# Optimization experiments

Hardware: AMD Instinct MI355X
Metric: run time of the kernel (lower is better)

Reference implementation:

```python
import jax, jax.numpy as jnp
import numpy as np

N = 100000   # nodes
E = 1600000  # edges per view
F = 256      # feature_dim
G = 512      # num graphs in batch
H, C = 2, 32 # heads, channels per head (GATConv(F, 32, heads=2))
EPS = 1e-5


def setup_inputs() -> dict:
    key = jax.random.key(0)
    ks = jax.random.split(key, 32)
    def w(i, shape, fan_in):
        return jax.random.normal(ks[i], shape, jnp.float32) / np.sqrt(fan_in)
    inp = {
        "x": jax.random.normal(ks[0], (N, F), jnp.float32),
        "edge_index_ast": jax.random.randint(ks[1], (2, E), 0, N),
        "edge_index_cfg": jax.random.randint(ks[2], (2, E), 0, N),
        "edge_index_pdg": jax.random.randint(ks[3], (2, E), 0, N),
        "batch": jnp.sort(jax.random.randint(ks[4], (N,), 0, G)),
        "num_graphs": G,
        # BatchNorm1d(feature_dim) affine params (training-mode batch stats)
        "bn_w": jnp.ones((F,), jnp.float32),
        "bn_b": jnp.zeros((F,), jnp.float32),
    }
    i = 5
    for v in ("ast", "cfg", "pdg"):
        inp[f"{v}_W"] = w(i, (F, H * C), F); i += 1
        inp[f"{v}_att_src"] = w(i, (H, C), C); i += 1
        inp[f"{v}_att_dst"] = w(i, (H, C), C); i += 1
        inp[f"{v}_bias"] = jnp.zeros((H * C,), jnp.float32)
    inp["g1_w"] = w(i, (64, 32), 64); i += 1
    inp["g1_b"] = jnp.zeros((32,), jnp.float32)
    inp["g2_w"] = w(i, (32, 3), 32); i += 1
    inp["g2_b"] = jnp.zeros((3,), jnp.float32)
    inp["c1_w"] = w(i, (64, 128), 64); i += 1
    inp["c1_b"] = jnp.zeros((128,), jnp.float32)
    inp["c2_w"] = w(i, (128, 64), 128); i += 1
    inp["c2_b"] = jnp.zeros((64,), jnp.float32)
    inp["c3_w"] = w(i, (64, 1), 64); i += 1
    inp["c3_b"] = jnp.zeros((1,), jnp.float32)
    return inp


def _gat(x, edge_index, W, att_src, att_dst, bias):
    """PyG GATConv (shared lin, add_self_loops=True, concat heads)."""
    n = x.shape[0]
    loops = jnp.arange(n)
    src = jnp.concatenate([edge_index[0], loops])
    dst = jnp.concatenate([edge_index[1], loops])
    h = (x @ W).reshape(n, H, C)                       # [N,H,C]
    a_src = jnp.sum(h * att_src, axis=-1)              # [N,H]
    a_dst = jnp.sum(h * att_dst, axis=-1)              # [N,H]
    e = jax.nn.leaky_relu(a_src[src] + a_dst[dst], 0.2)  # [Etot,H]
    m = jax.ops.segment_max(e, dst, num_segments=n)
    p = jnp.exp(e - m[dst])
    denom = jax.ops.segment_sum(p, dst, num_segments=n)
    alpha = p / (denom[dst] + 1e-16)                   # [Etot,H]
    out = jax.ops.segment_sum(h[src] * alpha[:, :, None], dst, num_segments=n)
    return out.reshape(n, H * C) + bias


def reference(x, edge_index_ast, edge_index_cfg, edge_index_pdg, batch, num_graphs,
              bn_w, bn_b,
              ast_W, ast_att_src, ast_att_dst, ast_bias,
              cfg_W, cfg_att_src, cfg_att_dst, cfg_bias,
              pdg_W, pdg_att_src, pdg_att_dst, pdg_bias,
              g1_w, g1_b, g2_w, g2_b,
              c1_w, c1_b, c2_w, c2_b, c3_w, c3_b):
    # input BatchNorm1d (training-mode batch statistics, biased variance)
    mu = x.mean(0)
    var = x.var(0)
    xn = (x - mu) / jnp.sqrt(var + EPS) * bn_w + bn_b

    h_ast = jax.ops.segment_max(jax.nn.elu(_gat(xn, edge_index_ast, ast_W, ast_att_src, ast_att_dst, ast_bias)), batch, num_segments=num_graphs)
    h_cfg = jax.ops.segment_max(jax.nn.elu(_gat(xn, edge_index_cfg, cfg_W, cfg_att_src, cfg_att_dst, cfg_bias)), batch, num_segments=num_graphs)
    h_pdg = jax.ops.segment_max(jax.nn.elu(_gat(xn, edge_index_pdg, pdg_W, pdg_att_src, pdg_att_dst, pdg_bias)), batch, num_segments=num_graphs)

    avg_view = (h_ast + h_cfg + h_pdg) / 3.0
    wts = jax.nn.softmax(jax.nn.relu(avg_view @ g1_w + g1_b) @ g2_w + g2_b, axis=-1)
    fused = wts[:, 0:1] * h_ast + wts[:, 1:2] * h_cfg + wts[:, 2:3] * h_pdg

    # classifier (dropout = identity at inference)
    z = jax.nn.relu(fused @ c1_w + c1_b)
    z = jax.nn.relu(z @ c2_w + c2_b)
    logits = (z @ c3_w + c3_b).reshape(-1)             # [G]
    return logits
```

## Files before the change

kernel.cpp:

```cpp
#include <hip/hip_runtime.h>
#include <hip/hip_bf16.h>
#include <hip/hip_fp16.h>

#define N_NODES 100000
#define N_EDGES 1600000
#define ETOT    (N_EDGES + N_NODES)
#define NE3     (3 * ETOT)
#define N3      (3 * N_NODES)
#define NF      256
#define NG      512
#define NHC     64
#define NOUT3   192
#define BN_EPS  1e-5f

#define NBUCK   586
#define NB1     1024
#define EGRAIN  20
#define ECHUNK  (256 * EGRAIN)
#define SCAN_N  (NBUCK * NB1)
#define ATT_NB  (N3 * 16 / 256)

typedef _Float16 f16x8 __attribute__((ext_vector_type(8)));
typedef float    f32x4 __attribute__((ext_vector_type(4)));

__device__ __forceinline__ unsigned fenc(float f){
  unsigned b = __float_as_uint(f);
  return (b & 0x80000000u) ? ~b : (b | 0x80000000u);
}
__device__ __forceinline__ float fdec(unsigned u){
  unsigned b = (u & 0x80000000u) ? (u & 0x7FFFFFFFu) : ~u;
  return __uint_as_float(b);
}
__device__ __forceinline__ float lrelu(float x){ return x > 0.f ? x : 0.2f * x; }
__device__ __forceinline__ float eluf(float x){ return x > 0.f ? x : (__expf(x) - 1.f); }

__global__ void k_init_pooled(unsigned* pooled){
  int i = blockIdx.x * 256 + threadIdx.x;
  if (i < 3 * NG * NHC) pooled[i] = 0x007FFFFFu;
}

#define STATS_NB ((N_NODES + 127) / 128)
__global__ __launch_bounds__(256) void k_pre(const float* __restrict__ x,
                                             float* __restrict__ sums, float* __restrict__ sumsq,
                                             const int* __restrict__ eA, const int* __restrict__ eC,
                                             const int* __restrict__ eP,
                                             int* __restrict__ gcounts){
  int t = threadIdx.x;
  if (blockIdx.x < STATS_NB){
    int r0 = blockIdx.x * 128;
    int rmax = N_NODES - r0; if (rmax > 128) rmax = 128;
    float s = 0.f, q = 0.f;
    for (int r = 0; r < rmax; ++r){
      float v = x[(size_t)(r0 + r) * NF + t];
      s += v; q += v * v;
    }
    atomicAdd(&sums[t], s);
    atomicAdd(&sumsq[t], q);
    return;
  }
  __shared__ int hist[NBUCK];
  int bi = blockIdx.x - STATS_NB;
  for (int b = t; b < NBUCK; b += 256) hist[b] = 0;
  __syncthreads();
  int base = bi * ECHUNK + t;
#pragma unroll
  for (int k = 0; k < EGRAIN; ++k){
    int i = base + k * 256;
    if (i < NE3){
      int v = i / ETOT; int j = i - v * ETOT;
      const int* ei = (v == 0) ? eA : (v == 1) ? eC : eP;
      int d = (j < N_EDGES) ? ei[N_EDGES + j] : (j - N_EDGES);
      int vd = v * N_NODES + d;
      atomicAdd(&hist[vd >> 9], 1);
    }
  }
  __syncthreads();
  for (int b = t; b < NBUCK; b += 256) gcounts[b * NB1 + bi] = hist[b];
}

__global__ __launch_bounds__(256) void k_prep2(const float* __restrict__ sums, const float* __restrict__ sumsq,
                                               const float* __restrict__ bn_w, const float* __restrict__ bn_b,
                                               const float* __restrict__ WA, const float* __restrict__ WC,
                                               const float* __restrict__ WP,
                                               __half* __restrict__ WpT, float* __restrict__ bp){
  __shared__ float red[256];
  int o = blockIdx.x;
  int v = o >> 6, oc = o & 63;
  const float* W = (v == 0) ? WA : (v == 1) ? WC : WP;
  int f = threadIdx.x;
  float mu  = sums[f]  * (1.f / N_NODES);
  float var = sumsq[f] * (1.f / N_NODES) - mu * mu;
  float sc  = bn_w[f] * rsqrtf(var + BN_EPS);
  float sh_ = bn_b[f] - mu * sc;
  float w = W[f * 64 + oc];
  WpT[(size_t)o * NF + f] = __float2half(w * sc);
  red[f] = sh_ * w;
  __syncthreads();
  for (int off = 128; off > 0; off >>= 1){
    if (f < off) red[f] += red[f + off];
    __syncthreads();
  }
  if (f == 0) bp[o] = red[0];
}

__global__ __launch_bounds__(256) void k_scan1(const int* __restrict__ cnt, int* __restrict__ out,
                                               int* __restrict__ bsum, int n){
  __shared__ int sh[256];
  int t = threadIdx.x; int base = blockIdx.x * 2048 + t * 8;
  int v[8]; int s = 0;
#pragma unroll
  for (int i = 0; i < 8; ++i){ v[i] = (base + i < n) ? cnt[base + i] : 0; s += v[i]; }
  sh[t] = s; __syncthreads();
  for (int off = 1; off < 256; off <<= 1){
    int xv = (t >= off) ? sh[t - off] : 0;
    __syncthreads();
    sh[t] += xv;
    __syncthreads();
  }
  int p = sh[t] - s;
  if (t == 255) bsum[blockIdx.x] = sh[255];
#pragma unroll
  for (int i = 0; i < 8; ++i){ if (base + i < n) out[base + i] = p; p += v[i]; }
}

__global__ __launch_bounds__(512) void k_scan2(int* __restrict__ bsum, int* __restrict__ total_out, int nb){
  __shared__ int sh[512];
  int t = threadIdx.x;
  int o = (t < nb) ? bsum[t] : 0;
  sh[t] = o; __syncthreads();
  for (int off = 1; off < 512; off <<= 1){
    int xv = (t >= off) ? sh[t - off] : 0;
    __syncthreads();
    sh[t] += xv;
    __syncthreads();
  }
  if (t < nb) bsum[t] = sh[t] - o;
  if (t == nb - 1) total_out[0] = sh[t];
}

__global__ __launch_bounds__(256) void k_scan3(int* __restrict__ out, const int* __restrict__ bsum, int n){
  int add = bsum[blockIdx.x];
  int base = blockIdx.x * 2048 + threadIdx.x * 8;
#pragma unroll
  for (int i = 0; i < 8; ++i) if (base + i < n) out[base + i] += add;
}

#define GBM 64
#define GEMM_NB ((N_NODES + GBM - 1) / GBM)
__global__ __launch_bounds__(256) void k_fused(const float* __restrict__ x,
                                               const __half* __restrict__ WpT, const float* __restrict__ bp,
                                               __half* __restrict__ h16,
                                               const int* __restrict__ eA, const int* __restrict__ eC,
                                               const int* __restrict__ eP,
                                               const int* __restrict__ gscan, int* __restrict__ packed){
  union U { _Float16 xs[64 * 256]; int pos[NBUCK]; };
  __shared__ U sm;
  int t = threadIdx.x;
  if (blockIdx.x >= GEMM_NB){
    int bi = blockIdx.x - GEMM_NB;
    for (int b = t; b < NBUCK; b += 256) sm.pos[b] = gscan[b * NB1 + bi];
    __syncthreads();
    int base = bi * ECHUNK + t;
#pragma unroll
    for (int k = 0; k < EGRAIN; ++k){
      int i = base + k * 256;
      if (i < NE3){
        int v = i / ETOT; int j = i - v * ETOT;
        const int* ei = (v == 0) ? eA : (v == 1) ? eC : eP;
        int s, d;
        if (j < N_EDGES){ s = ei[j]; d = ei[N_EDGES + j]; } else { s = j - N_EDGES; d = s; }
        int vd = v * N_NODES + d;
        int p = atomicAdd(&sm.pos[vd >> 9], 1);
        packed[p] = s | ((vd & 511) << 17);
      }
    }
    return;
  }
  int m0 = blockIdx.x * GBM;
#pragma unroll
  for (int k = 0; k < 8; ++k){
    int G = t + k * 256;
    int row = G >> 5, g = G & 31;
    int grow = m0 + row; if (grow >= N_NODES) grow = N_NODES - 1;
    const float4* src = (const float4*)(x + (size_t)grow * NF + ((g ^ (row & 7)) << 3));
    float4 lo = src[0], hi = src[1];
    f16x8 h;
    h[0]=(_Float16)lo.x; h[1]=(_Float16)lo.y; h[2]=(_Float16)lo.z; h[3]=(_Float16)lo.w;
    h[4]=(_Float16)hi.x; h[5]=(_Float16)hi.y; h[6]=(_Float16)hi.z; h[7]=(_Float16)hi.w;
    *(f16x8*)&sm.xs[(size_t)G << 3] = h;
  }
  __syncthreads();
  int lane = t & 63, w = t >> 6;
  int lr = lane & 15, lk = lane >> 4;
  int colb = w * 48;
  f32x4 acc[4][3];
#pragma unroll
  for (int mt = 0; mt < 4; ++mt)
#pragma unroll
    for (int ct = 0; ct < 3; ++ct) acc[mt][ct] = (f32x4){0.f, 0.f, 0.f, 0.f};
  float bpv[3];
#pragma unroll
  for (int ct = 0; ct < 3; ++ct) bpv[ct] = bp[colb + ct * 16 + lr];
#pragma unroll
  for (int kk = 0; kk < 8; ++kk){
    int khalf = kk * 32 + lk * 8;
    f16x8 av[4];
#pragma unroll
    for (int mt = 0; mt < 4; ++mt){
      int row = mt * 16 + lr;
      av[mt] = *(const f16x8*)&sm.xs[row * 256 + (khalf ^ ((row & 7) << 3))];
    }
    f16x8 bv[3];
#pragma unroll
    for (int ct = 0; ct < 3; ++ct){
      int col = colb + ct * 16 + lr;
      bv[ct] = *(const f16x8*)(const void*)(WpT + (size_t)col * NF + khalf);
    }
#pragma unroll
    for (int mt = 0; mt < 4; ++mt)
#pragma unroll
      for (int ct = 0; ct < 3; ++ct)
        acc[mt][ct] = __builtin_amdgcn_mfma_f32_16x16x32_f16(av[mt], bv[ct], acc[mt][ct], 0, 0, 0);
  }
#pragma unroll
  for (int mt = 0; mt < 4; ++mt){
#pragma unroll
    for (int r = 0; r < 4; ++r){
      int row = m0 + mt * 16 + lk * 4 + r;
      if (row < N_NODES){
#pragma unroll
        for (int ct = 0; ct < 3; ++ct)
          h16[(size_t)row * NOUT3 + colb + ct * 16 + lr] = __float2half(acc[mt][ct][r] + bpv[ct]);
      }
    }
  }
}

__global__ __launch_bounds__(256) void k_build(const int* __restrict__ gscan, const int* __restrict__ packed,
                                               int* __restrict__ entries, int* __restrict__ offsets){
  __shared__ int hist2[512];
  __shared__ int sh[256];
  int b = blockIdx.x, t = threadIdx.x;
  int base = gscan[b * NB1];
  int end  = (b == NBUCK - 1) ? NE3 : gscan[(b + 1) * NB1];
  hist2[t * 2] = 0; hist2[t * 2 + 1] = 0;
  __syncthreads();
  for (int i = base + t; i < end; i += 256)
    atomicAdd(&hist2[(packed[i] >> 17) & 511], 1);
  __syncthreads();
  int s0 = hist2[t * 2], s1 = hist2[t * 2 + 1];
  int tot = s0 + s1;
  sh[t] = tot; __syncthreads();
  for (int off = 1; off < 256; off <<= 1){
    int xv = (t >= off) ? sh[t - off] : 0;
    __syncthreads();
    sh[t] += xv;
    __syncthreads();
  }
  int p = sh[t] - tot;
  hist2[t * 2]     = p;
  hist2[t * 2 + 1] = p + s0;
  __syncthreads();
#pragma unroll
  for (int i = 0; i < 2; ++i){
    int vd = (b << 9) + t * 2 + i;
    if (vd < N3) offsets[vd] = base + hist2[t * 2 + i];
  }
  if (b == NBUCK - 1 && t == 0) offsets[N3] = NE3;
  __syncthreads();
  for (int i = base + t; i < end; i += 256){
    int pk = packed[i];
    int low = (pk >> 17) & 511;
    int pos = atomicAdd(&hist2[low], 1);
    entries[base + pos] = pk & 0x1FFFF;
  }
}

__global__ __launch_bounds__(256) void k_att(const __half* __restrict__ h16,
                                             const float* __restrict__ asA, const float* __restrict__ adA,
                                             const float* __restrict__ asC, const float* __restrict__ adC,
                                             const float* __restrict__ asP, const float* __restrict__ adP,
                                             float* __restrict__ a_src, float* __restrict__ a_dst,
                                             unsigned* __restrict__ gpart){
  __shared__ unsigned samax[6];
  int t = threadIdx.x;
  if (t < 6) samax[t] = 0u;
  __syncthreads();
  int gt = blockIdx.x * 256 + t;
  int g = gt >> 4; int lid = gt & 15;
  int v = g / N_NODES; int n = g - v * N_NODES;
  const float* As = (v == 0) ? asA : (v == 1) ? asC : asP;
  const float* Ad = (v == 0) ? adA : (v == 1) ? adC : adP;
  const __half2* hp = (const __half2*)(h16 + (size_t)n * NOUT3 + v * 64 + lid * 4);
  float2 fa = __half22float2(hp[0]);
  float2 fb = __half22float2(hp[1]);
  float4 s4 = *(const float4*)(As + lid * 4);
  float4 d4 = *(const float4*)(Ad + lid * 4);
  float rs = fa.x*s4.x + fa.y*s4.y + fb.x*s4.z + fb.y*s4.w;
  float rd = fa.x*d4.x + fa.y*d4.y + fb.x*d4.z + fb.y*d4.w;
  rs += __shfl_xor(rs, 1); rd += __shfl_xor(rd, 1);
  rs += __shfl_xor(rs, 2); rd += __shfl_xor(rd, 2);
  rs += __shfl_xor(rs, 4); rd += __shfl_xor(rd, 4);
  if ((lid & 7) == 0){
    int h = lid >> 3;
    a_src[g * 2 + h] = rs;
    a_dst[g * 2 + h] = rd;
    atomicMax(&samax[v * 2 + h], fenc(rs));
  }
  __syncthreads();
  if (t < 6) gpart[blockIdx.x * 6 + t] = samax[t];
}

__global__ __launch_bounds__(256) void k_amax(const unsigned* __restrict__ gpart, unsigned* __restrict__ amax){
  __shared__ unsigned sm[6];
  int t = threadIdx.x;
  if (t < 6) sm[t] = 0u;
  __syncthreads();
  unsigned m[6] = {0u, 0u, 0u, 0u, 0u, 0u};
  for (int bi = t; bi < ATT_NB; bi += 256){
    const unsigned* p = gpart + (size_t)bi * 6;
#pragma unroll
    for (int k = 0; k < 6; ++k) m[k] = max(m[k], p[k]);
  }
#pragma unroll
  for (int k = 0; k < 6; ++k) atomicMax(&sm[k], m[k]);
  __syncthreads();
  if (t < 6) amax[t] = sm[t];
}

__global__ __launch_bounds__(256) void k_gather(const int* __restrict__ entries, const int* __restrict__ offsets,
                                                const float* __restrict__ a_src, const float* __restrict__ a_dst,
                                                const unsigned* __restrict__ amax,
                                                const __half* __restrict__ h16,
                                                const float* __restrict__ bA, const float* __restrict__ bC,
                                                const float* __restrict__ bP,
                                                const int* __restrict__ batch, unsigned* __restrict__ pooled){
  __shared__ unsigned red[64];
  __shared__ int kmin, kmax;
  int t = threadIdx.x;
  if (t == 0){ kmin = 0x7FFFFFFF; kmax = -1; }
  if (t < 64) red[t] = 0u;
  __syncthreads();
  int grp = t >> 4;
  int lid = t & 15;
  int g = blockIdx.x * 16 + grp;
  int v = g / N_NODES; int n = g - v * N_NODES;
  int vN = v * N_NODES;
  float ad0 = a_dst[g*2+0], ad1 = a_dst[g*2+1];
  float m0 = lrelu(fdec(amax[v*2+0]) + ad0);
  float m1 = lrelu(fdec(amax[v*2+1]) + ad1);
  int beg = offsets[g], end = offsets[g+1];
  int len = end - beg;
  float ax = 0.f, ay = 0.f, az = 0.f, aw = 0.f;
  float den0 = 0.f, den1 = 0.f;
  const __half* hbase = h16 + v * 64 + lid * 4;
  for (int c0 = 0; c0 < len; c0 += 16){
    int nc = len - c0; if (nc > 16) nc = 16;
    int s_ = 0; float p0 = 0.f, p1 = 0.f;
    if (lid < nc){
      s_ = entries[beg + c0 + lid];
      float2 ap = *(const float2*)(a_src + (size_t)(vN + s_) * 2);
      p0 = __expf(lrelu(ap.x + ad0) - m0);
      p1 = __expf(lrelu(ap.y + ad1) - m1);
    }
    den0 += p0; den1 += p1;
    for (int k = 0; k < nc; k += 4){
      uint2 r[4]; float pav[4], pbv[4];
#pragma unroll
      for (int j = 0; j < 4; ++j){
        int kk = k + j;
        int sk = __shfl(s_, kk, 16);
        r[j] = *(const uint2*)(hbase + (size_t)sk * NOUT3);
        pav[j] = __shfl(p0, kk, 16);
        pbv[j] = __shfl(p1, kk, 16);
      }
#pragma unroll
      for (int j = 0; j < 4; ++j){
        int kk = k + j;
        if (kk < nc){
          float ph = (lid < 8) ? pav[j] : pbv[j];
          float2 fa2 = __half22float2(*(__half2*)&r[j].x);
          float2 fb2 = __half22float2(*(__half2*)&r[j].y);
          ax += ph * fa2.x; ay += ph * fa2.y; az += ph * fb2.x; aw += ph * fb2.y;
        }
      }
    }
  }
#pragma unroll
  for (int msk = 1; msk < 16; msk <<= 1){
    den0 += __shfl_xor(den0, msk);
    den1 += __shfl_xor(den1, msk);
  }
  float den = ((lid < 8) ? den0 : den1) + 1e-16f;
  const float* bias = (v == 0) ? bA : (v == 1) ? bC : bP;
  float4 b4 = *(const float4*)(bias + lid * 4);
  unsigned e0u = fenc(eluf(ax / den + b4.x));
  unsigned e1u = fenc(eluf(ay / den + b4.y));
  unsigned e2u = fenc(eluf(az / den + b4.z));
  unsigned e3u = fenc(eluf(aw / den + b4.w));
  int key = v * NG + batch[n];
  if (lid == 0){ atomicMin(&kmin, key); atomicMax(&kmax, key); }
  atomicMax(&red[lid*4+0], e0u); atomicMax(&red[lid*4+1], e1u);
  atomicMax(&red[lid*4+2], e2u); atomicMax(&red[lid*4+3], e3u);
  __syncthreads();
  if (kmin == kmax){
    if (t < 64) atomicMax(&pooled[(size_t)kmin * 64 + t], red[t]);
  } else {
    unsigned* pp = pooled + (size_t)key * 64 + lid * 4;
    atomicMax(pp+0, e0u); atomicMax(pp+1, e1u); atomicMax(pp+2, e2u); atomicMax(pp+3, e3u);
  }
}

__global__ __launch_bounds__(64) void k_head(const unsigned* __restrict__ pooled,
                                             const float* __restrict__ g1w, const float* __restrict__ g1b,
                                             const float* __restrict__ g2w, const float* __restrict__ g2b,
                                             const float* __restrict__ c1w, const float* __restrict__ c1b,
                                             const float* __restrict__ c2w, const float* __restrict__ c2b,
                                             const float* __restrict__ c3w, const float* __restrict__ c3b,
                                             float* __restrict__ out){
  __shared__ float s1[64];
  __shared__ float s2[128];
  __shared__ float sw[3];
  int g = blockIdx.x, l = threadIdx.x;
  float ha = fdec(pooled[(size_t)g * 64 + l]);
  float hc = fdec(pooled[(size_t)(NG + g) * 64 + l]);
  float hp = fdec(pooled[(size_t)(2 * NG + g) * 64 + l]);
  s1[l] = (ha + hc + hp) * (1.f / 3.f);
  __syncthreads();
  float r1 = 0.f;
  if (l < 32){
    r1 = g1b[l];
    for (int i = 0; i < 64; ++i) r1 += s1[i] * g1w[i * 32 + l];
    r1 = fmaxf(r1, 0.f);
  }
  __syncthreads();
  if (l < 32) s2[l] = r1;
  __syncthreads();
  if (l < 3){
    float tv = g2b[l];
    for (int i = 0; i < 32; ++i) tv += s2[i] * g2w[i * 3 + l];
    sw[l] = tv;
  }
  __syncthreads();
  float t0 = sw[0], t1 = sw[1], t2 = sw[2];
  float mx = fmaxf(t0, fmaxf(t1, t2));
  float w0 = __expf(t0 - mx), w1 = __expf(t1 - mx), w2 = __expf(t2 - mx);
  float wsum = w0 + w1 + w2;
  float fused = (w0 * ha + w1 * hc + w2 * hp) / wsum;
  __syncthreads();
  s1[l] = fused;
  __syncthreads();
  float za = c1b[l], zb = c1b[64 + l];
  for (int i = 0; i < 64; ++i){
    float f = s1[i];
    za += f * c1w[i * 128 + l];
    zb += f * c1w[i * 128 + 64 + l];
  }
  za = fmaxf(za, 0.f); zb = fmaxf(zb, 0.f);
  s2[l] = za; s2[64 + l] = zb;
  __syncthreads();
  float z2 = c2b[l];
  for (int i = 0; i < 128; ++i) z2 += s2[i] * c2w[i * 64 + l];
  z2 = fmaxf(z2, 0.f);
  float prod = z2 * c3w[l];
  for (int off = 32; off > 0; off >>= 1) prod += __shfl_down(prod, off);
  if (l == 0) out[g] = prod + c3b[0];
}

extern "C" void kernel_launch(void* const* d_in, const int* in_sizes, int n_in,
                              void* d_out, int out_size, void* d_ws, size_t ws_size,
                              hipStream_t stream){
  const float* x    = (const float*)d_in[0];
  const int* eA     = (const int*)d_in[1];
  const int* eC     = (const int*)d_in[2];
  const int* eP     = (const int*)d_in[3];
  const int* batch  = (const int*)d_in[4];
  const float* bn_w = (const float*)d_in[6];
  const float* bn_b = (const float*)d_in[7];
  const float* WA   = (const float*)d_in[8];
  const float* asA  = (const float*)d_in[9];
  const float* adA  = (const float*)d_in[10];
  const float* bA   = (const float*)d_in[11];
  const float* WC   = (const float*)d_in[12];
  const float* asC  = (const float*)d_in[13];
  const float* adC  = (const float*)d_in[14];
  const float* bC   = (const float*)d_in[15];
  const float* WP   = (const float*)d_in[16];
  const float* asP  = (const float*)d_in[17];
  const float* adP  = (const float*)d_in[18];
  const float* bP   = (const float*)d_in[19];
  const float* g1w  = (const float*)d_in[20];
  const float* g1b  = (const float*)d_in[21];
  const float* g2w  = (const float*)d_in[22];
  const float* g2b  = (const float*)d_in[23];
  const float* c1w  = (const float*)d_in[24];
  const float* c1b  = (const float*)d_in[25];
  const float* c2w  = (const float*)d_in[26];
  const float* c2b  = (const float*)d_in[27];
  const float* c3w  = (const float*)d_in[28];
  const float* c3b  = (const float*)d_in[29];
  float* out = (float*)d_out;

  char* wptr = (char*)d_ws;
  auto alloc = [&](size_t bytes) -> void* {
    void* p = (void*)wptr;
    wptr += (bytes + 255) & ~(size_t)255;
    return p;
  };
  float*    sums    = (float*)   alloc((size_t)NF * 4);
  float*    sumsq   = (float*)   alloc((size_t)NF * 4);
  size_t zbytes = (size_t)(wptr - (char*)sums);
  int*      gcounts = (int*)     alloc((size_t)SCAN_N * 4);
  int*      gscan   = (int*)     alloc((size_t)SCAN_N * 4);
  int*      offsets = (int*)     alloc(((size_t)N3 + 1) * 4);
  __half*   WpT     = (__half*)  alloc((size_t)NOUT3 * NF * 2);
  float*    bp      = (float*)   alloc((size_t)NOUT3 * 4);
  __half*   h16     = (__half*)  alloc((size_t)N_NODES * NOUT3 * 2);
  float*    a_src   = (float*)   alloc((size_t)N3 * 2 * 4);
  float*    a_dst   = (float*)   alloc((size_t)N3 * 2 * 4);
  int*      packed  = (int*)     alloc((size_t)NE3 * 4);
  int*      entries = (int*)     alloc((size_t)NE3 * 4);
  unsigned* pooled  = (unsigned*)alloc((size_t)3 * NG * NHC * 4);
  unsigned* gpart   = (unsigned*)alloc((size_t)ATT_NB * 6 * 4);
  unsigned* amax    = (unsigned*)alloc((size_t)64 * 4);
  int*      bsum    = (int*)     alloc((size_t)512 * 4);
  int*      scrtot  = (int*)     alloc((size_t)64 * 4);

  hipMemsetAsync(sums, 0, zbytes, stream);
  k_init_pooled<<<(3 * NG * NHC + 255) / 256, 256, 0, stream>>>(pooled);
  k_pre<<<STATS_NB + NB1, 256, 0, stream>>>(x, sums, sumsq, eA, eC, eP, gcounts);
  k_prep2<<<NOUT3, 256, 0, stream>>>(sums, sumsq, bn_w, bn_b, WA, WC, WP, WpT, bp);
  int nb_sc = (SCAN_N + 2047) / 2048;
  k_scan1<<<nb_sc, 256, 0, stream>>>(gcounts, gscan, bsum, SCAN_N);
  k_scan2<<<1, 512, 0, stream>>>(bsum, scrtot, nb_sc);
  k_scan3<<<nb_sc, 256, 0, stream>>>(gscan, bsum, SCAN_N);
  k_fused<<<GEMM_NB + NB1, 256, 0, stream>>>(x, WpT, bp, h16, eA, eC, eP, gscan, packed);
  k_att<<<ATT_NB, 256, 0, stream>>>(h16, asA, adA, asC, adC, asP, adP, a_src, a_dst, gpart);
  k_amax<<<1, 256, 0, stream>>>(gpart, amax);
  k_build<<<NBUCK, 256, 0, stream>>>(gscan, packed, entries, offsets);
  k_gather<<<N3 / 16, 256, 0, stream>>>(entries, offsets, a_src, a_dst, amax, h16, bA, bC, bP, batch, pooled);
  k_head<<<NG, 64, 0, stream>>>(pooled, g1w, g1b, g2w, g2b, c1w, c1b, c2w, c2b, c3w, c3b, out);
}
```

Measured before the change: 377.5 us.

## Precompute edge softmax weights in CSR build and narrow gather to 8 lanes

The CSR build kernel now computes each edge's unnormalized attention weights for both heads, using a_src, a_dst and the global max. It stores them as packed fp16 next to the source index in an 8-byte entry. The gather kernel then skips the random a_src lookup and the exp work, and uses 8 lanes per destination node with 16-byte feature loads instead of 16 lanes with 8-byte loads. The trade-off is doubled edge-entry traffic, fp16 rounding of the attention weights, and the exp plus random a_src access moving into the build kernel.

```diff
diff --git a/kernel.cpp b/kernel.cpp
--- a/kernel.cpp
+++ b/kernel.cpp
@@ -233,46 +233,6 @@
           h16[(size_t)row * NOUT3 + colb + ct * 16 + lr] = __float2half(acc[mt][ct][r] + bpv[ct]);
       }
     }
-  }
-}
-
-__global__ __launch_bounds__(256) void k_build(const int* __restrict__ gscan, const int* __restrict__ packed,
-                                               int* __restrict__ entries, int* __restrict__ offsets){
-  __shared__ int hist2[512];
-  __shared__ int sh[256];
-  int b = blockIdx.x, t = threadIdx.x;
-  int base = gscan[b * NB1];
-  int end  = (b == NBUCK - 1) ? NE3 : gscan[(b + 1) * NB1];
-  hist2[t * 2] = 0; hist2[t * 2 + 1] = 0;
-  __syncthreads();
-  for (int i = base + t; i < end; i += 256)
-    atomicAdd(&hist2[(packed[i] >> 17) & 511], 1);
-  __syncthreads();
-  int s0 = hist2[t * 2], s1 = hist2[t * 2 + 1];
-  int tot = s0 + s1;
-  sh[t] = tot; __syncthreads();
-  for (int off = 1; off < 256; off <<= 1){
-    int xv = (t >= off) ? sh[t - off] : 0;
-    __syncthreads();
-    sh[t] += xv;
-    __syncthreads();
-  }
-  int p = sh[t] - tot;
-  hist2[t * 2]     = p;
-  hist2[t * 2 + 1] = p + s0;
-  __syncthreads();
-#pragma unroll
-  for (int i = 0; i < 2; ++i){
-    int vd = (b << 9) + t * 2 + i;
-    if (vd < N3) offsets[vd] = base + hist2[t * 2 + i];
-  }
-  if (b == NBUCK - 1 && t == 0) offsets[N3] = NE3;
-  __syncthreads();
-  for (int i = base + t; i < end; i += 256){
-    int pk = packed[i];
-    int low = (pk >> 17) & 511;
-    int pos = atomicAdd(&hist2[low], 1);
-    entries[base + pos] = pk & 0x1FFFF;
   }
 }
 
@@ -328,9 +288,62 @@
   if (t < 6) amax[t] = sm[t];
 }
 
-__global__ __launch_bounds__(256) void k_gather(const int* __restrict__ entries, const int* __restrict__ offsets,
-                                                const float* __restrict__ a_src, const float* __restrict__ a_dst,
-                                                const unsigned* __restrict__ amax,
+__global__ __launch_bounds__(256) void k_build(const int* __restrict__ gscan, const int* __restrict__ packed,
+                                               const float* __restrict__ a_src, const float* __restrict__ a_dst,
+                                               const unsigned* __restrict__ amax,
+                                               uint2* __restrict__ ep, int* __restrict__ offsets){
+  __shared__ int hist2[512];
+  __shared__ int sh[256];
+  __shared__ float sam[6];
+  int b = blockIdx.x, t = threadIdx.x;
+  if (t < 6) sam[t] = fdec(amax[t]);
+  int base = gscan[b * NB1];
+  int end  = (b == NBUCK - 1) ? NE3 : gscan[(b + 1) * NB1];
+  hist2[t * 2] = 0; hist2[t * 2 + 1] = 0;
+  __syncthreads();
+  for (int i = base + t; i < end; i += 256)
+    atomicAdd(&hist2[(packed[i] >> 17) & 511], 1);
+  __syncthreads();
+  int s0 = hist2[t * 2], s1 = hist2[t * 2 + 1];
+  int tot = s0 + s1;
+  sh[t] = tot; __syncthreads();
+  for (int off = 1; off < 256; off <<= 1){
+    int xv = (t >= off) ? sh[t - off] : 0;
+    __syncthreads();
+    sh[t] += xv;
+    __syncthreads();
+  }
+  int p = sh[t] - tot;
+  hist2[t * 2]     = p;
+  hist2[t * 2 + 1] = p + s0;
+  __syncthreads();
+#pragma unroll
+  for (int i = 0; i < 2; ++i){
+    int vd = (b << 9) + t * 2 + i;
+    if (vd < N3) offsets[vd] = base + hist2[t * 2 + i];
+  }
+  if (b == NBUCK - 1 && t == 0) offsets[N3] = NE3;
+  __syncthreads();
+  for (int i = base + t; i < end; i += 256){
+    int pk = packed[i];
+    int low = (pk >> 17) & 511;
+    int s = pk & 0x1FFFF;
+    int vd = (b << 9) + low;
+    int v = (vd >= 2 * N_NODES) ? 2 : (vd >= N_NODES) ? 1 : 0;
+    float2 ad = *(const float2*)(a_dst + (size_t)vd * 2);
+    float2 as = *(const float2*)(a_src + (size_t)(v * N_NODES + s) * 2);
+    float m0 = lrelu(sam[v * 2 + 0] + ad.x);
+    float m1 = lrelu(sam[v * 2 + 1] + ad.y);
+    float p0 = __expf(lrelu(as.x + ad.x) - m0);
+    float p1 = __expf(lrelu(as.y + ad.y) - m1);
+    unsigned pu = (unsigned)__half_as_ushort(__float2half(p0))
+                | ((unsigned)__half_as_ushort(__float2half(p1)) << 16);
+    int pos = atomicAdd(&hist2[low], 1);
+    ep[base + pos] = make_uint2((unsigned)s, pu);
+  }
+}
+
+__global__ __launch_bounds__(256) void k_gather(const uint2* __restrict__ ep, const int* __restrict__ offsets,
                                                 const __half* __restrict__ h16,
                                                 const float* __restrict__ bA, const float* __restrict__ bC,
                                                 const float* __restrict__ bP,
@@ -341,73 +354,70 @@
   if (t == 0){ kmin = 0x7FFFFFFF; kmax = -1; }
   if (t < 64) red[t] = 0u;
   __syncthreads();
-  int grp = t >> 4;
-  int lid = t & 15;
-  int g = blockIdx.x * 16 + grp;
+  int grp = t >> 3;
+  int lid = t & 7;
+  int g = blockIdx.x * 32 + grp;
   int v = g / N_NODES; int n = g - v * N_NODES;
-  int vN = v * N_NODES;
-  float ad0 = a_dst[g*2+0], ad1 = a_dst[g*2+1];
-  float m0 = lrelu(fdec(amax[v*2+0]) + ad0);
-  float m1 = lrelu(fdec(amax[v*2+1]) + ad1);
   int beg = offsets[g], end = offsets[g+1];
   int len = end - beg;
-  float ax = 0.f, ay = 0.f, az = 0.f, aw = 0.f;
+  float acc[8];
+#pragma unroll
+  for (int e2 = 0; e2 < 8; ++e2) acc[e2] = 0.f;
   float den0 = 0.f, den1 = 0.f;
-  const __half* hbase = h16 + v * 64 + lid * 4;
-  for (int c0 = 0; c0 < len; c0 += 16){
-    int nc = len - c0; if (nc > 16) nc = 16;
-    int s_ = 0; float p0 = 0.f, p1 = 0.f;
+  const __half* hbase = h16 + v * 64 + lid * 8;
+  for (int c0 = 0; c0 < len; c0 += 8){
+    int nc = len - c0; if (nc > 8) nc = 8;
+    int s_ = 0; unsigned pu_ = 0u;
     if (lid < nc){
-      s_ = entries[beg + c0 + lid];
-      float2 ap = *(const float2*)(a_src + (size_t)(vN + s_) * 2);
-      p0 = __expf(lrelu(ap.x + ad0) - m0);
-      p1 = __expf(lrelu(ap.y + ad1) - m1);
-    }
-    den0 += p0; den1 += p1;
+      uint2 e = ep[beg + c0 + lid];
+      s_ = (int)e.x; pu_ = e.y;
+    }
+    den0 += __half2float(__ushort_as_half((unsigned short)(pu_ & 0xFFFFu)));
+    den1 += __half2float(__ushort_as_half((unsigned short)(pu_ >> 16)));
     for (int k = 0; k < nc; k += 4){
-      uint2 r[4]; float pav[4], pbv[4];
+      f16x8 r[4]; float pa[4];
 #pragma unroll
       for (int j = 0; j < 4; ++j){
         int kk = k + j;
-        int sk = __shfl(s_, kk, 16);
-        r[j] = *(const uint2*)(hbase + (size_t)sk * NOUT3);
-        pav[j] = __shfl(p0, kk, 16);
-        pbv[j] = __shfl(p1, kk, 16);
+        int sk = __shfl(s_, kk, 8);
+        unsigned pk_ = (unsigned)__shfl((int)pu_, kk, 8);
+        r[j] = *(const f16x8*)(hbase + (size_t)sk * NOUT3);
+        unsigned sel = (lid < 4) ? (pk_ & 0xFFFFu) : (pk_ >> 16);
+        pa[j] = __half2float(__ushort_as_half((unsigned short)sel));
       }
 #pragma unroll
       for (int j = 0; j < 4; ++j){
-        int kk = k + j;
-        if (kk < nc){
-          float ph = (lid < 8) ? pav[j] : pbv[j];
-          float2 fa2 = __half22float2(*(__half2*)&r[j].x);
-          float2 fb2 = __half22float2(*(__half2*)&r[j].y);
-          ax += ph * fa2.x; ay += ph * fa2.y; az += ph * fb2.x; aw += ph * fb2.y;
-        }
+#pragma unroll
+        for (int e2 = 0; e2 < 8; ++e2)
+          acc[e2] = fmaf(pa[j], (float)r[j][e2], acc[e2]);
       }
     }
   }
 #pragma unroll
-  for (int msk = 1; msk < 16; msk <<= 1){
+  for (int msk = 1; msk < 8; msk <<= 1){
     den0 += __shfl_xor(den0, msk);
     den1 += __shfl_xor(den1, msk);
   }
-  float den = ((lid < 8) ? den0 : den1) + 1e-16f;
+  float den = ((lid < 4) ? den0 : den1) + 1e-16f;
   const float* bias = (v == 0) ? bA : (v == 1) ? bC : bP;
-  float4 b4 = *(const float4*)(bias + lid * 4);
-  unsigned e0u = fenc(eluf(ax / den + b4.x));
-  unsigned e1u = fenc(eluf(ay / den + b4.y));
-  unsigned e2u = fenc(eluf(az / den + b4.z));
-  unsigned e3u = fenc(eluf(aw / den + b4.w));
+  float4 b4a = *(const float4*)(bias + lid * 8);
+  float4 b4b = *(const float4*)(bias + lid * 8 + 4);
+  float bv[8] = {b4a.x, b4a.y, b4a.z, b4a.w, b4b.x, b4b.y, b4b.z, b4b.w};
+  unsigned eo[8];
+#pragma unroll
+  for (int e2 = 0; e2 < 8; ++e2)
+    eo[e2] = fenc(eluf(acc[e2] / den + bv[e2]));
   int key = v * NG + batch[n];
   if (lid == 0){ atomicMin(&kmin, key); atomicMax(&kmax, key); }
-  atomicMax(&red[lid*4+0], e0u); atomicMax(&red[lid*4+1], e1u);
-  atomicMax(&red[lid*4+2], e2u); atomicMax(&red[lid*4+3], e3u);
+#pragma unroll
+  for (int e2 = 0; e2 < 8; ++e2) atomicMax(&red[lid * 8 + e2], eo[e2]);
   __syncthreads();
   if (kmin == kmax){
     if (t < 64) atomicMax(&pooled[(size_t)kmin * 64 + t], red[t]);
   } else {
-    unsigned* pp = pooled + (size_t)key * 64 + lid * 4;
-    atomicMax(pp+0, e0u); atomicMax(pp+1, e1u); atomicMax(pp+2, e2u); atomicMax(pp+3, e3u);
+    unsigned* pp = pooled + (size_t)key * 64 + lid * 8;
+#pragma unroll
+    for (int e2 = 0; e2 < 8; ++e2) atomicMax(pp + e2, eo[e2]);
   }
 }
 
@@ -519,7 +529,7 @@
   float*    a_src   = (float*)   alloc((size_t)N3 * 2 * 4);
   float*    a_dst   = (float*)   alloc((size_t)N3 * 2 * 4);
   int*      packed  = (int*)     alloc((size_t)NE3 * 4);
-  int*      entries = (int*)     alloc((size_t)NE3 * 4);
+  uint2*    ep      = (uint2*)   alloc((size_t)NE3 * 8);
   unsigned* pooled  = (unsigned*)alloc((size_t)3 * NG * NHC * 4);
   unsigned* gpart   = (unsigned*)alloc((size_t)ATT_NB * 6 * 4);
   unsigned* amax    = (unsigned*)alloc((size_t)64 * 4);
@@ -537,7 +547,7 @@
   k_fused<<<GEMM_NB + NB1, 256, 0, stream>>>(x, WpT, bp, h16, eA, eC, eP, gscan, packed);
   k_att<<<ATT_NB, 256, 0, stream>>>(h16, asA, adA, asC, adC, asP, adP, a_src, a_dst, gpart);
   k_amax<<<1, 256, 0, stream>>>(gpart, amax);
-  k_build<<<NBUCK, 256, 0, stream>>>(gscan, packed, entries, offsets);
-  k_gather<<<N3 / 16, 256, 0, stream>>>(entries, offsets, a_src, a_dst, amax, h16, bA, bC, bP, batch, pooled);
+  k_build<<<NBUCK, 256, 0, stream>>>(gscan, packed, a_src, a_dst, amax, ep, offsets);
+  k_gather<<<N3 / 32, 256, 0, stream>>>(ep, offsets, h16, bA, bC, bP, batch, pooled);
   k_head<<<NG, 64, 0, stream>>>(pooled, g1w, g1b, g2w, g2b, c1w, c1b, c2w, c2b, c3w, c3b, out);
 }
```

New measurement: 553.7 us. 1.47x slower.

## Precompute fp16 attention weights in CSR build and pack with source index

Applied to the files above, without the earlier changes.

The CSR build kernel now computes the unnormalized softmax weight exp(lrelu(a_src+a_dst)-m) for each edge. It stores the two heads as packed fp16 next to the source index in a uint2 entry. The gather kernel no longer loads a_src/a_dst or evaluates exp; it reads the packed pair and unpacks the weight. The build kernel moves to 512 threads so each thread owns one histogram bin, and the gather inner loop is unrolled by 8 without the per-edge bounds check, relying on zero weights in the padding lanes. The cost shifts to build, which now does the random a_src gathers, and the fp16 weights may underflow or lose precision.

```diff
diff --git a/kernel.cpp b/kernel.cpp
--- a/kernel.cpp
+++ b/kernel.cpp
@@ -233,46 +233,6 @@
           h16[(size_t)row * NOUT3 + colb + ct * 16 + lr] = __float2half(acc[mt][ct][r] + bpv[ct]);
       }
     }
-  }
-}
-
-__global__ __launch_bounds__(256) void k_build(const int* __restrict__ gscan, const int* __restrict__ packed,
-                                               int* __restrict__ entries, int* __restrict__ offsets){
-  __shared__ int hist2[512];
-  __shared__ int sh[256];
-  int b = blockIdx.x, t = threadIdx.x;
-  int base = gscan[b * NB1];
-  int end  = (b == NBUCK - 1) ? NE3 : gscan[(b + 1) * NB1];
-  hist2[t * 2] = 0; hist2[t * 2 + 1] = 0;
-  __syncthreads();
-  for (int i = base + t; i < end; i += 256)
-    atomicAdd(&hist2[(packed[i] >> 17) & 511], 1);
-  __syncthreads();
-  int s0 = hist2[t * 2], s1 = hist2[t * 2 + 1];
-  int tot = s0 + s1;
-  sh[t] = tot; __syncthreads();
-  for (int off = 1; off < 256; off <<= 1){
-    int xv = (t >= off) ? sh[t - off] : 0;
-    __syncthreads();
-    sh[t] += xv;
-    __syncthreads();
-  }
-  int p = sh[t] - tot;
-  hist2[t * 2]     = p;
-  hist2[t * 2 + 1] = p + s0;
-  __syncthreads();
-#pragma unroll
-  for (int i = 0; i < 2; ++i){
-    int vd = (b << 9) + t * 2 + i;
-    if (vd < N3) offsets[vd] = base + hist2[t * 2 + i];
-  }
-  if (b == NBUCK - 1 && t == 0) offsets[N3] = NE3;
-  __syncthreads();
-  for (int i = base + t; i < end; i += 256){
-    int pk = packed[i];
-    int low = (pk >> 17) & 511;
-    int pos = atomicAdd(&hist2[low], 1);
-    entries[base + pos] = pk & 0x1FFFF;
   }
 }
 
@@ -328,9 +288,56 @@
   if (t < 6) amax[t] = sm[t];
 }
 
-__global__ __launch_bounds__(256) void k_gather(const int* __restrict__ entries, const int* __restrict__ offsets,
-                                                const float* __restrict__ a_src, const float* __restrict__ a_dst,
-                                                const unsigned* __restrict__ amax,
+__global__ __launch_bounds__(512) void k_build(const int* __restrict__ gscan, const int* __restrict__ packed,
+                                               const float* __restrict__ a_src, const float* __restrict__ a_dst,
+                                               const unsigned* __restrict__ amax,
+                                               uint2* __restrict__ ep, int* __restrict__ offsets){
+  __shared__ int hist2[512];
+  __shared__ int sh[512];
+  __shared__ float sam[6];
+  int b = blockIdx.x, t = threadIdx.x;
+  if (t < 6) sam[t] = fdec(amax[t]);
+  int base = gscan[b * NB1];
+  int end  = (b == NBUCK - 1) ? NE3 : gscan[(b + 1) * NB1];
+  hist2[t] = 0;
+  __syncthreads();
+  for (int i = base + t; i < end; i += 512)
+    atomicAdd(&hist2[(packed[i] >> 17) & 511], 1);
+  __syncthreads();
+  int cnt = hist2[t];
+  sh[t] = cnt; __syncthreads();
+  for (int off = 1; off < 512; off <<= 1){
+    int xv = (t >= off) ? sh[t - off] : 0;
+    __syncthreads();
+    sh[t] += xv;
+    __syncthreads();
+  }
+  int excl = sh[t] - cnt;
+  hist2[t] = excl;
+  int vd0 = (b << 9) + t;
+  if (vd0 < N3) offsets[vd0] = base + excl;
+  if (b == NBUCK - 1 && t == 0) offsets[N3] = NE3;
+  __syncthreads();
+  for (int i = base + t; i < end; i += 512){
+    int pk = packed[i];
+    int low = (pk >> 17) & 511;
+    int s = pk & 0x1FFFF;
+    int vd = (b << 9) + low;
+    int v = (vd >= 2 * N_NODES) ? 2 : (vd >= N_NODES) ? 1 : 0;
+    float2 ad = *(const float2*)(a_dst + (size_t)vd * 2);
+    float2 as = *(const float2*)(a_src + (size_t)(v * N_NODES + s) * 2);
+    float m0 = lrelu(sam[v * 2 + 0] + ad.x);
+    float m1 = lrelu(sam[v * 2 + 1] + ad.y);
+    float p0 = __expf(lrelu(as.x + ad.x) - m0);
+    float p1 = __expf(lrelu(as.y + ad.y) - m1);
+    unsigned pu = (unsigned)__half_as_ushort(__float2half(p0))
+                | ((unsigned)__half_as_ushort(__float2half(p1)) << 16);
+    int pos = atomicAdd(&hist2[low], 1);
+    ep[base + pos] = make_uint2((unsigned)s, pu);
+  }
+}
+
+__global__ __launch_bounds__(256) void k_gather(const uint2* __restrict__ ep, const int* __restrict__ offsets,
                                                 const __half* __restrict__ h16,
                                                 const float* __restrict__ bA, const float* __restrict__ bC,
                                                 const float* __restrict__ bP,
@@ -345,10 +352,6 @@
   int lid = t & 15;
   int g = blockIdx.x * 16 + grp;
   int v = g / N_NODES; int n = g - v * N_NODES;
-  int vN = v * N_NODES;
-  float ad0 = a_dst[g*2+0], ad1 = a_dst[g*2+1];
-  float m0 = lrelu(fdec(amax[v*2+0]) + ad0);
-  float m1 = lrelu(fdec(amax[v*2+1]) + ad1);
   int beg = offsets[g], end = offsets[g+1];
   int len = end - beg;
   float ax = 0.f, ay = 0.f, az = 0.f, aw = 0.f;
@@ -356,33 +359,30 @@
   const __half* hbase = h16 + v * 64 + lid * 4;
   for (int c0 = 0; c0 < len; c0 += 16){
     int nc = len - c0; if (nc > 16) nc = 16;
-    int s_ = 0; float p0 = 0.f, p1 = 0.f;
+    int s_ = 0; unsigned pu_ = 0u;
     if (lid < nc){
-      s_ = entries[beg + c0 + lid];
-      float2 ap = *(const float2*)(a_src + (size_t)(vN + s_) * 2);
-      p0 = __expf(lrelu(ap.x + ad0) - m0);
-      p1 = __expf(lrelu(ap.y + ad1) - m1);
-    }
-    den0 += p0; den1 += p1;
-    for (int k = 0; k < nc; k += 4){
-      uint2 r[4]; float pav[4], pbv[4];
-#pragma unroll
-      for (int j = 0; j < 4; ++j){
+      uint2 e = ep[beg + c0 + lid];
+      s_ = (int)e.x; pu_ = e.y;
+    }
+    den0 += __half2float(__ushort_as_half((unsigned short)(pu_ & 0xFFFFu)));
+    den1 += __half2float(__ushort_as_half((unsigned short)(pu_ >> 16)));
+    for (int k = 0; k < nc; k += 8){
+      uint2 r[8]; float pa[8];
+#pragma unroll
+      for (int j = 0; j < 8; ++j){
         int kk = k + j;
         int sk = __shfl(s_, kk, 16);
+        unsigned pk_ = (unsigned)__shfl((int)pu_, kk, 16);
         r[j] = *(const uint2*)(hbase + (size_t)sk * NOUT3);
-        pav[j] = __shfl(p0, kk, 16);
-        pbv[j] = __shfl(p1, kk, 16);
+        unsigned sel = (lid < 8) ? (pk_ & 0xFFFFu) : (pk_ >> 16);
+        pa[j] = __half2float(__ushort_as_half((unsigned short)sel));
       }
 #pragma unroll
-      for (int j = 0; j < 4; ++j){
-        int kk = k + j;
-        if (kk < nc){
-          float ph = (lid < 8) ? pav[j] : pbv[j];
-          float2 fa2 = __half22float2(*(__half2*)&r[j].x);
-          float2 fb2 = __half22float2(*(__half2*)&r[j].y);
-          ax += ph * fa2.x; ay += ph * fa2.y; az += ph * fb2.x; aw += ph * fb2.y;
-        }
+      for (int j = 0; j < 8; ++j){
+        float2 fa2 = __half22float2(*(__half2*)&r[j].x);
+        float2 fb2 = __half22float2(*(__half2*)&r[j].y);
+        ax = fmaf(pa[j], fa2.x, ax); ay = fmaf(pa[j], fa2.y, ay);
+        az = fmaf(pa[j], fb2.x, az); aw = fmaf(pa[j], fb2.y, aw);
       }
     }
   }
@@ -519,7 +519,7 @@
   float*    a_src   = (float*)   alloc((size_t)N3 * 2 * 4);
   float*    a_dst   = (float*)   alloc((size_t)N3 * 2 * 4);
   int*      packed  = (int*)     alloc((size_t)NE3 * 4);
-  int*      entries = (int*)     alloc((size_t)NE3 * 4);
+  uint2*    ep      = (uint2*)   alloc((size_t)NE3 * 8);
   unsigned* pooled  = (unsigned*)alloc((size_t)3 * NG * NHC * 4);
   unsigned* gpart   = (unsigned*)alloc((size_t)ATT_NB * 6 * 4);
   unsigned* amax    = (unsigned*)alloc((size_t)64 * 4);
@@ -537,7 +537,7 @@
   k_fused<<<GEMM_NB + NB1, 256, 0, stream>>>(x, WpT, bp, h16, eA, eC, eP, gscan, packed);
   k_att<<<ATT_NB, 256, 0, stream>>>(h16, asA, adA, asC, adC, asP, adP, a_src, a_dst, gpart);
   k_amax<<<1, 256, 0, stream>>>(gpart, amax);
-  k_build<<<NBUCK, 256, 0, stream>>>(gscan, packed, entries, offsets);
-  k_gather<<<N3 / 16, 256, 0, stream>>>(entries, offsets, a_src, a_dst, amax, h16, bA, bC, bP, batch, pooled);
+  k_build<<<NBUCK, 512, 0, stream>>>(gscan, packed, a_src, a_dst, amax, ep, offsets);
+  k_gather<<<N3 / 16, 256, 0, stream>>>(ep, offsets, h16, bA, bC, bP, batch, pooled);
   k_head<<<NG, 64, 0, stream>>>(pooled, g1w, g1b, g2w, g2b, c1w, c1b, c2w, c2b, c3w, c3b, out);
 }
```

Measured after the change: 411.6 us. 1.09x slower.
